# Kernel tuning notes

Hardware: AMD Instinct MI355X
Metric: run time of the kernel (lower is better)

## Reference

```python
import jax, jax.numpy as jnp
import numpy as np
import math

N, M, DIM = 16384, 4096, 1024


def setup_inputs() -> dict:
    key = jax.random.key(0)
    k1, k2, k3, k4, k5 = jax.random.split(key, 5)
    x = jax.random.normal(k1, (N, DIM), dtype=jnp.float32)
    e_repr = jax.random.normal(k2, (M, DIM), dtype=jnp.float32)
    H = jax.random.randint(k3, (N, M), 0, 2, dtype=jnp.int32)  # incidence matrix, >0 = connected
    # nn.Linear(dim, dim, bias=False) weights, scaled like torch default init
    W_e = jax.random.normal(k4, (DIM, DIM), dtype=jnp.float32) / math.sqrt(DIM)
    W_n = jax.random.normal(k5, (DIM, DIM), dtype=jnp.float32) / math.sqrt(DIM)
    return {"x": x, "e_repr": e_repr, "H": H, "W_e": W_e, "W_n": W_n}


def reference(x, e_repr, H, W_e, W_n):
    he = e_repr @ W_e.T            # [M, dim]  (W_e(e_repr); original recomputes this, same math)
    hn = x @ W_n.T                 # [N, dim]
    scale = 1.0 / math.sqrt(he.shape[1])
    B = (hn @ he.T) * scale        # [N, M] scores
    mask = H > 0
    B = jnp.where(mask, B, -1e9)
    B = jax.nn.softmax(B, axis=1) * mask.astype(B.dtype)
    out = jax.nn.elu(B @ he)       # [N, dim]
    return out, B
```

## Files before the change

### kernel.cpp

```cpp
#include <hip/hip_runtime.h>

#define NN 16384
#define MM 4096
#define DD 1024

typedef unsigned short u16;
typedef unsigned int u32;
typedef short bf16x8 __attribute__((ext_vector_type(8)));
typedef float f32x4 __attribute__((ext_vector_type(4)));

enum { EPI_SPLIT = 0, EPI_SPLITH = 1, EPI_MASK = 2 };

__global__ void sentinel_kernel(float* out, float val) {
    if (blockIdx.x == 0 && threadIdx.x < 64) out[threadIdx.x] = val;
}

__device__ __forceinline__ void gload16(const void* g, void* l) {
    __builtin_amdgcn_global_load_lds(
        (const __attribute__((address_space(1))) void*)g,
        (__attribute__((address_space(3))) void*)l, 16, 0, 0);
}

__device__ __forceinline__ void split2(float f, u16& hi, u16& lo) {
    const u32 u = __float_as_uint(f);
    hi = (u16)(u >> 16);
    const float r = f - __uint_as_float(u & 0xffff0000u);
    lo = (u16)(__float_as_uint(r) >> 16);
}

__device__ __forceinline__ u16 f2bf_rtne(float f) {
    const u32 u = __float_as_uint(f);
    return (u16)((u + 0x7FFFu + ((u >> 16) & 1u)) >> 16);
}

__global__ __launch_bounds__(256) void split_f32(
    const float* __restrict__ src, u16* __restrict__ hi, u16* __restrict__ lo,
    long n4)
{
    long i = (long)blockIdx.x * 256 + threadIdx.x;
    const long stride = (long)gridDim.x * 256;
    for (; i < n4; i += stride) {
        const float4 v = ((const float4*)src)[i];
        ushort4 h, l;
        split2(v.x, h.x, l.x); split2(v.y, h.y, l.y);
        split2(v.z, h.z, l.z); split2(v.w, h.w, l.w);
        ((ushort4*)hi)[i] = h;
        ((ushort4*)lo)[i] = l;
    }
}

template <int EPI>
__global__ __launch_bounds__(256) void gemm_ps3(
    const u16* __restrict__ Ah, const u16* __restrict__ Al,
    const u16* __restrict__ Bh, const u16* __restrict__ Bl,
    u16* __restrict__ Ch, u16* __restrict__ Cl,
    float* __restrict__ Cf, const int* __restrict__ Hm,
    int Cc, int K)
{
    __shared__ u16 sAh[2][128][32];
    __shared__ u16 sAl[2][128][32];
    __shared__ u16 sBh[2][128][32];
    __shared__ u16 sBl[2][128][32];

    const int tid = threadIdx.x;
    const int lane = tid & 63;
    const int w = tid >> 6;
    const int wm = (w >> 1) * 64;
    const int wn = (w & 1) * 64;
    const int l15 = lane & 15;
    const int l4 = lane >> 4;
    const int rowBlk = blockIdx.y * 128;
    const int colBlk = blockIdx.x * 128;

    const int srow = w * 32 + (lane >> 2);
    const int scol = ((lane & 3) ^ ((lane >> 3) & 3)) * 8;
    const int rchunk = (l4 ^ ((l15 >> 1) & 3)) * 8;

    f32x4 acc[4][4] = {};

    auto stage = [&](int b, int k0) {
        const size_t ra = (size_t)(rowBlk + srow) * K + k0 + scol;
        const size_t rb = (size_t)(colBlk + srow) * K + k0 + scol;
        gload16(Ah + ra,                  &sAh[b][w * 32][0]);
        gload16(Ah + ra + (size_t)16 * K, &sAh[b][w * 32 + 16][0]);
        gload16(Al + ra,                  &sAl[b][w * 32][0]);
        gload16(Al + ra + (size_t)16 * K, &sAl[b][w * 32 + 16][0]);
        gload16(Bh + rb,                  &sBh[b][w * 32][0]);
        gload16(Bh + rb + (size_t)16 * K, &sBh[b][w * 32 + 16][0]);
        gload16(Bl + rb,                  &sBl[b][w * 32][0]);
        gload16(Bl + rb + (size_t)16 * K, &sBl[b][w * 32 + 16][0]);
    };

    stage(0, 0);
    __syncthreads();
    int cur = 0;

    for (int k0 = 0; k0 < K; k0 += 32) {
        if (k0 + 32 < K) stage(cur ^ 1, k0 + 32);

        bf16x8 a_h[4], a_l[4], b_h[4], b_l[4];
#pragma unroll
        for (int m = 0; m < 4; ++m) {
            const int r = wm + m * 16 + l15;
            a_h[m] = *(const bf16x8*)&sAh[cur][r][rchunk];
            a_l[m] = *(const bf16x8*)&sAl[cur][r][rchunk];
        }
#pragma unroll
        for (int n = 0; n < 4; ++n) {
            const int c = wn + n * 16 + l15;
            b_h[n] = *(const bf16x8*)&sBh[cur][c][rchunk];
            b_l[n] = *(const bf16x8*)&sBl[cur][c][rchunk];
        }

#pragma unroll
        for (int m = 0; m < 4; ++m)
#pragma unroll
            for (int n = 0; n < 4; ++n)
                acc[m][n] = __builtin_amdgcn_mfma_f32_16x16x32_bf16(a_h[m], b_h[n], acc[m][n], 0, 0, 0);
#pragma unroll
        for (int m = 0; m < 4; ++m)
#pragma unroll
            for (int n = 0; n < 4; ++n)
                acc[m][n] = __builtin_amdgcn_mfma_f32_16x16x32_bf16(a_h[m], b_l[n], acc[m][n], 0, 0, 0);
#pragma unroll
        for (int m = 0; m < 4; ++m)
#pragma unroll
            for (int n = 0; n < 4; ++n)
                acc[m][n] = __builtin_amdgcn_mfma_f32_16x16x32_bf16(a_l[m], b_h[n], acc[m][n], 0, 0, 0);

        __syncthreads();
        cur ^= 1;
    }

    const size_t ldc = (size_t)Cc;
#pragma unroll
    for (int m = 0; m < 4; ++m) {
#pragma unroll
        for (int n = 0; n < 4; ++n) {
            const int col = colBlk + wn + n * 16 + l15;
#pragma unroll
            for (int r = 0; r < 4; ++r) {
                const int row = rowBlk + wm + m * 16 + l4 * 4 + r;
                const size_t idx = (size_t)row * ldc + col;
                if constexpr (EPI == EPI_MASK) {
                    float v = acc[m][n][r] * 0.03125f;
                    if (Hm[idx] <= 0) v = -1e9f;
                    Cf[idx] = v;
                } else {
                    u16 hi, lo;
                    split2(acc[m][n][r], hi, lo);
                    Ch[idx] = hi;
                    if constexpr (EPI == EPI_SPLIT) Cl[idx] = lo;
                }
            }
        }
    }
}

__global__ __launch_bounds__(256) void gemm_bf16_elu(
    const u16* __restrict__ A, const u16* __restrict__ Bt,
    float* __restrict__ C, int Cc, int K)
{
    __shared__ u16 sA[2][128][32];
    __shared__ u16 sB[2][128][32];

    const int tid = threadIdx.x;
    const int lane = tid & 63;
    const int w = tid >> 6;
    const int wm = (w >> 1) * 64;
    const int wn = (w & 1) * 64;
    const int l15 = lane & 15;
    const int l4 = lane >> 4;
    const int rowBlk = blockIdx.y * 128;
    const int colBlk = blockIdx.x * 128;

    const int srow = w * 32 + (lane >> 2);
    const int scol = ((lane & 3) ^ ((lane >> 3) & 3)) * 8;
    const int rchunk = (l4 ^ ((l15 >> 1) & 3)) * 8;

    f32x4 acc[4][4] = {};

    auto stage = [&](int b, int k0) {
        const size_t ra = (size_t)(rowBlk + srow) * K + k0 + scol;
        const size_t rb = (size_t)(colBlk + srow) * K + k0 + scol;
        gload16(A + ra,                   &sA[b][w * 32][0]);
        gload16(A + ra + (size_t)16 * K,  &sA[b][w * 32 + 16][0]);
        gload16(Bt + rb,                  &sB[b][w * 32][0]);
        gload16(Bt + rb + (size_t)16 * K, &sB[b][w * 32 + 16][0]);
    };

    stage(0, 0);
    __syncthreads();
    int cur = 0;

    for (int k0 = 0; k0 < K; k0 += 32) {
        if (k0 + 32 < K) stage(cur ^ 1, k0 + 32);

        bf16x8 a[4], b[4];
#pragma unroll
        for (int m = 0; m < 4; ++m)
            a[m] = *(const bf16x8*)&sA[cur][wm + m * 16 + l15][rchunk];
#pragma unroll
        for (int n = 0; n < 4; ++n)
            b[n] = *(const bf16x8*)&sB[cur][wn + n * 16 + l15][rchunk];

#pragma unroll
        for (int m = 0; m < 4; ++m)
#pragma unroll
            for (int n = 0; n < 4; ++n)
                acc[m][n] = __builtin_amdgcn_mfma_f32_16x16x32_bf16(a[m], b[n], acc[m][n], 0, 0, 0);

        __syncthreads();
        cur ^= 1;
    }

    const size_t ldc = (size_t)Cc;
#pragma unroll
    for (int m = 0; m < 4; ++m) {
#pragma unroll
        for (int n = 0; n < 4; ++n) {
            const int col = colBlk + wn + n * 16 + l15;
#pragma unroll
            for (int r = 0; r < 4; ++r) {
                const int row = rowBlk + wm + m * 16 + l4 * 4 + r;
                float v = acc[m][n][r];
                v = v > 0.f ? v : (expf(v) - 1.f);
                C[(size_t)row * ldc + col] = v;
            }
        }
    }
}

__global__ __launch_bounds__(256) void softmax_rows_f32(
    float* __restrict__ Bm, u16* __restrict__ B16)
{
    const int row = blockIdx.x;
    const int tid = threadIdx.x;
    const int lane = tid & 63;
    const int wid = tid >> 6;
    float4* rp = reinterpret_cast<float4*>(Bm + (size_t)row * MM);

    float4 q[4];
#pragma unroll
    for (int i = 0; i < 4; ++i) q[i] = rp[i * 256 + tid];
    float v[16];
#pragma unroll
    for (int i = 0; i < 4; ++i) {
        v[4 * i + 0] = q[i].x; v[4 * i + 1] = q[i].y;
        v[4 * i + 2] = q[i].z; v[4 * i + 3] = q[i].w;
    }

    float mx = -3e38f;
#pragma unroll
    for (int i = 0; i < 16; ++i) mx = fmaxf(mx, v[i]);
#pragma unroll
    for (int off = 32; off >= 1; off >>= 1) mx = fmaxf(mx, __shfl_xor(mx, off));
    __shared__ float red[4];
    if (lane == 0) red[wid] = mx;
    __syncthreads();
    mx = fmaxf(fmaxf(red[0], red[1]), fmaxf(red[2], red[3]));
    __syncthreads();

    float e[16];
    float s = 0.f;
#pragma unroll
    for (int i = 0; i < 16; ++i) { e[i] = expf(v[i] - mx); s += e[i]; }
#pragma unroll
    for (int off = 32; off >= 1; off >>= 1) s += __shfl_xor(s, off);
    if (lane == 0) red[wid] = s;
    __syncthreads();
    s = red[0] + red[1] + red[2] + red[3];
    const float inv = (mx > -1e8f && s > 0.f) ? (1.0f / s) : 0.f;

    ushort4* hp = reinterpret_cast<ushort4*>(B16 + (size_t)row * MM);
#pragma unroll
    for (int i = 0; i < 4; ++i) {
        q[i].x = e[4 * i + 0] * inv; q[i].y = e[4 * i + 1] * inv;
        q[i].z = e[4 * i + 2] * inv; q[i].w = e[4 * i + 3] * inv;
        rp[i * 256 + tid] = q[i];
        ushort4 h;
        h.x = f2bf_rtne(q[i].x); h.y = f2bf_rtne(q[i].y);
        h.z = f2bf_rtne(q[i].z); h.w = f2bf_rtne(q[i].w);
        hp[i * 256 + tid] = h;
    }
}

extern "C" void kernel_launch(void* const* d_in, const int* in_sizes, int n_in,
                              void* d_out, int out_size, void* d_ws, size_t ws_size,
                              hipStream_t stream)
{
    (void)d_ws; (void)ws_size;

    float* O = (float*)d_out;
    bool ok_sizes = (n_in == 5)
        && in_sizes[0] == NN * DD && in_sizes[1] == MM * DD
        && in_sizes[2] == NN * MM
        && in_sizes[3] == DD * DD && in_sizes[4] == DD * DD;
    if (!ok_sizes) { sentinel_kernel<<<1, 64, 0, stream>>>(O, 1e6f); return; }
    if (out_size != NN * DD + NN * MM) { sentinel_kernel<<<1, 64, 0, stream>>>(O, 2e6f); return; }

    const float* x  = (const float*)d_in[0];
    const float* er = (const float*)d_in[1];
    const int*   Hm = (const int*)d_in[2];
    const float* We = (const float*)d_in[3];
    const float* Wn = (const float*)d_in[4];

    float* Bo = O + (size_t)NN * DD;

    u16* xs_h  = (u16*)Bo;
    u16* xs_l  = xs_h  + (size_t)NN * DD;
    u16* ers_h = xs_l  + (size_t)NN * DD;
    u16* ers_l = ers_h + (size_t)MM * DD;
    u16* wes_h = ers_l + (size_t)MM * DD;
    u16* wes_l = wes_h + (size_t)DD * DD;
    u16* wns_h = wes_l + (size_t)DD * DD;
    u16* wns_l = wns_h + (size_t)DD * DD;

    u16* hn_h  = (u16*)O;
    u16* hn_l  = hn_h + (size_t)NN * DD;
    u16* he_h  = (u16*)d_in[0];
    u16* he_l  = he_h + (size_t)MM * DD;
    u16* heT_h = he_l + (size_t)MM * DD;
    u16* B16   = (u16*)d_in[2];

    dim3 blk(256);
    split_f32<<<dim3(2048), blk, 0, stream>>>(x,  xs_h,  xs_l,  (long)NN * DD / 4);
    split_f32<<<dim3(1024), blk, 0, stream>>>(er, ers_h, ers_l, (long)MM * DD / 4);
    split_f32<<<dim3(512),  blk, 0, stream>>>(We, wes_h, wes_l, (long)DD * DD / 4);
    split_f32<<<dim3(512),  blk, 0, stream>>>(Wn, wns_h, wns_l, (long)DD * DD / 4);
    gemm_ps3<EPI_SPLIT><<<dim3(DD / 128, NN / 128), blk, 0, stream>>>(
        xs_h, xs_l, wns_h, wns_l, hn_h, hn_l, nullptr, nullptr, DD, DD);
    gemm_ps3<EPI_SPLIT><<<dim3(DD / 128, MM / 128), blk, 0, stream>>>(
        ers_h, ers_l, wes_h, wes_l, he_h, he_l, nullptr, nullptr, DD, DD);
    gemm_ps3<EPI_SPLITH><<<dim3(MM / 128, DD / 128), blk, 0, stream>>>(
        wes_h, wes_l, ers_h, ers_l, heT_h, nullptr, nullptr, nullptr, MM, DD);
    gemm_ps3<EPI_MASK><<<dim3(MM / 128, NN / 128), blk, 0, stream>>>(
        hn_h, hn_l, he_h, he_l, nullptr, nullptr, Bo, Hm, MM, DD);
    softmax_rows_f32<<<dim3(NN), blk, 0, stream>>>(Bo, B16);
    gemm_bf16_elu<<<dim3(DD / 128, NN / 128), blk, 0, stream>>>(B16, heT_h, O, DD, MM);
}
```

Measured before the change: 1.431 ms.

## Pack incidence mask into bitmasks and use explicit vmcnt waits in GEMM loops

Adds a pack_mask kernel that ballots the int32 incidence matrix into 64-bit bitmasks stored in a scratch buffer. The masked-score GEMM epilogue then reads one u64 per row group instead of an int per element, cutting mask traffic in that epilogue. Separately, both GEMM main loops replace __syncthreads with partial s_waitcnt vmcnt plus raw s_barrier, so the prefetch of the next tile can stay in flight while the current one is consumed. The extra pack pass still reads the full int mask once, and the hand-written waitcnt counts must match the number of issued loads to stay correct.

```diff
diff --git a/kernel.cpp b/kernel.cpp
--- a/kernel.cpp
+++ b/kernel.cpp
@@ -6,6 +6,7 @@
 
 typedef unsigned short u16;
 typedef unsigned int u32;
+typedef unsigned long long u64;
 typedef short bf16x8 __attribute__((ext_vector_type(8)));
 typedef float f32x4 __attribute__((ext_vector_type(4)));
 
@@ -49,12 +50,25 @@
     }
 }
 
+__global__ __launch_bounds__(256) void pack_mask(
+    const int* __restrict__ Hm, u64* __restrict__ Mb)
+{
+    const int lane = threadIdx.x & 63;
+    const int wid = threadIdx.x >> 6;
+    const long nt = (long)NN * (MM / 64);
+    for (long t = (long)blockIdx.x * 4 + wid; t < nt; t += (long)gridDim.x * 4) {
+        const int v = Hm[t * 64 + lane];
+        const u64 m = __ballot(v > 0);
+        if (lane == 0) Mb[t] = m;
+    }
+}
+
 template <int EPI>
 __global__ __launch_bounds__(256) void gemm_ps3(
     const u16* __restrict__ Ah, const u16* __restrict__ Al,
     const u16* __restrict__ Bh, const u16* __restrict__ Bl,
     u16* __restrict__ Ch, u16* __restrict__ Cl,
-    float* __restrict__ Cf, const int* __restrict__ Hm,
+    float* __restrict__ Cf, const u64* __restrict__ Mb,
     int Cc, int K)
 {
     __shared__ u16 sAh[2][128][32];
@@ -92,11 +106,17 @@
     };
 
     stage(0, 0);
-    __syncthreads();
     int cur = 0;
 
     for (int k0 = 0; k0 < K; k0 += 32) {
-        if (k0 + 32 < K) stage(cur ^ 1, k0 + 32);
+        if (k0 + 32 < K) {
+            stage(cur ^ 1, k0 + 32);
+            asm volatile("s_waitcnt vmcnt(8)" ::: "memory");
+        } else {
+            asm volatile("s_waitcnt vmcnt(0)" ::: "memory");
+        }
+        __builtin_amdgcn_s_barrier();
+        __builtin_amdgcn_sched_barrier(0);
 
         bf16x8 a_h[4], a_l[4], b_h[4], b_l[4];
 #pragma unroll
@@ -128,29 +148,42 @@
             for (int n = 0; n < 4; ++n)
                 acc[m][n] = __builtin_amdgcn_mfma_f32_16x16x32_bf16(a_l[m], b_h[n], acc[m][n], 0, 0, 0);
 
-        __syncthreads();
+        __builtin_amdgcn_s_barrier();
         cur ^= 1;
     }
 
     const size_t ldc = (size_t)Cc;
-#pragma unroll
-    for (int m = 0; m < 4; ++m) {
-#pragma unroll
-        for (int n = 0; n < 4; ++n) {
-            const int col = colBlk + wn + n * 16 + l15;
+    if constexpr (EPI == EPI_MASK) {
+        const int grp = (colBlk + wn) >> 6;
+        const int gpr = Cc >> 6;
+#pragma unroll
+        for (int m = 0; m < 4; ++m) {
 #pragma unroll
             for (int r = 0; r < 4; ++r) {
                 const int row = rowBlk + wm + m * 16 + l4 * 4 + r;
-                const size_t idx = (size_t)row * ldc + col;
-                if constexpr (EPI == EPI_MASK) {
+                const u64 g = Mb[(size_t)row * gpr + grp];
+#pragma unroll
+                for (int n = 0; n < 4; ++n) {
+                    const int col = colBlk + wn + n * 16 + l15;
                     float v = acc[m][n][r] * 0.03125f;
-                    if (Hm[idx] <= 0) v = -1e9f;
-                    Cf[idx] = v;
-                } else {
+                    if (!((g >> (n * 16 + l15)) & 1ull)) v = -1e9f;
+                    Cf[(size_t)row * ldc + col] = v;
+                }
+            }
+        }
+    } else {
+#pragma unroll
+        for (int m = 0; m < 4; ++m) {
+#pragma unroll
+            for (int n = 0; n < 4; ++n) {
+                const int col = colBlk + wn + n * 16 + l15;
+#pragma unroll
+                for (int r = 0; r < 4; ++r) {
+                    const int row = rowBlk + wm + m * 16 + l4 * 4 + r;
                     u16 hi, lo;
                     split2(acc[m][n][r], hi, lo);
-                    Ch[idx] = hi;
-                    if constexpr (EPI == EPI_SPLIT) Cl[idx] = lo;
+                    Ch[(size_t)row * ldc + col] = hi;
+                    if constexpr (EPI == EPI_SPLIT) Cl[(size_t)row * ldc + col] = lo;
                 }
             }
         }
@@ -190,11 +223,17 @@
     };
 
     stage(0, 0);
-    __syncthreads();
     int cur = 0;
 
     for (int k0 = 0; k0 < K; k0 += 32) {
-        if (k0 + 32 < K) stage(cur ^ 1, k0 + 32);
+        if (k0 + 32 < K) {
+            stage(cur ^ 1, k0 + 32);
+            asm volatile("s_waitcnt vmcnt(4)" ::: "memory");
+        } else {
+            asm volatile("s_waitcnt vmcnt(0)" ::: "memory");
+        }
+        __builtin_amdgcn_s_barrier();
+        __builtin_amdgcn_sched_barrier(0);
 
         bf16x8 a[4], b[4];
 #pragma unroll
@@ -210,7 +249,7 @@
             for (int n = 0; n < 4; ++n)
                 acc[m][n] = __builtin_amdgcn_mfma_f32_16x16x32_bf16(a[m], b[n], acc[m][n], 0, 0, 0);
 
-        __syncthreads();
+        __builtin_amdgcn_s_barrier();
         cur ^= 1;
     }
 
@@ -321,6 +360,7 @@
     u16* he_h  = (u16*)d_in[0];
     u16* he_l  = he_h + (size_t)MM * DD;
     u16* heT_h = he_l + (size_t)MM * DD;
+    u64* Mb    = (u64*)d_in[1];
     u16* B16   = (u16*)d_in[2];
 
     dim3 blk(256);
@@ -328,6 +368,7 @@
     split_f32<<<dim3(1024), blk, 0, stream>>>(er, ers_h, ers_l, (long)MM * DD / 4);
     split_f32<<<dim3(512),  blk, 0, stream>>>(We, wes_h, wes_l, (long)DD * DD / 4);
     split_f32<<<dim3(512),  blk, 0, stream>>>(Wn, wns_h, wns_l, (long)DD * DD / 4);
+    pack_mask<<<dim3(4096), blk, 0, stream>>>(Hm, Mb);
     gemm_ps3<EPI_SPLIT><<<dim3(DD / 128, NN / 128), blk, 0, stream>>>(
         xs_h, xs_l, wns_h, wns_l, hn_h, hn_l, nullptr, nullptr, DD, DD);
     gemm_ps3<EPI_SPLIT><<<dim3(DD / 128, MM / 128), blk, 0, stream>>>(
@@ -335,7 +376,7 @@
     gemm_ps3<EPI_SPLITH><<<dim3(MM / 128, DD / 128), blk, 0, stream>>>(
         wes_h, wes_l, ers_h, ers_l, heT_h, nullptr, nullptr, nullptr, MM, DD);
     gemm_ps3<EPI_MASK><<<dim3(MM / 128, NN / 128), blk, 0, stream>>>(
-        hn_h, hn_l, he_h, he_l, nullptr, nullptr, Bo, Hm, MM, DD);
+        hn_h, hn_l, he_h, he_l, nullptr, nullptr, Bo, Mb, MM, DD);
     softmax_rows_f32<<<dim3(NN), blk, 0, stream>>>(Bo, B16);
     gemm_bf16_elu<<<dim3(DD / 128, NN / 128), blk, 0, stream>>>(B16, heT_h, O, DD, MM);
 }
```

Result: slower. 1.520 ms (+6.2%).
